# Performance work log

Measured on AMD Instinct MI355X. Metric: run time of the kernel, lower is better.

The kernel has to match this reference:

```python
import jax, jax.numpy as jnp
import numpy as np

B = 8192
D = 4096  # input_size == hidden_size (required by the module's forward)
H = 4096


def setup_inputs() -> dict:
    key = jax.random.key(0)
    ks = jax.random.split(key, 14)
    s = 0.02
    inp = {
        "input": jax.random.normal(ks[0], (B, D), dtype=jnp.float32),
        "hidden_state": jax.random.normal(ks[1], (B, H), dtype=jnp.float32),
        # torch nn.Linear weights: [out_features, in_features]
        "w_ir": jax.random.normal(ks[2], (H, D), dtype=jnp.float32) * s,
        "b_ir": jax.random.normal(ks[3], (H,), dtype=jnp.float32) * s,
        "w_iz": jax.random.normal(ks[4], (H, D), dtype=jnp.float32) * s,
        "b_iz": jax.random.normal(ks[5], (H,), dtype=jnp.float32) * s,
        "w_in": jax.random.normal(ks[6], (H, D), dtype=jnp.float32) * s,
        "b_in": jax.random.normal(ks[7], (H,), dtype=jnp.float32) * s,
        "w_hr": jax.random.normal(ks[8], (H, H), dtype=jnp.float32) * s,
        "b_hr": jax.random.normal(ks[9], (H,), dtype=jnp.float32) * s,
        "w_hz": jax.random.normal(ks[10], (H, H), dtype=jnp.float32) * s,
        "b_hz": jax.random.normal(ks[11], (H,), dtype=jnp.float32) * s,
        "w_hn": jax.random.normal(ks[12], (H, H), dtype=jnp.float32) * s,
        "b_hn": jax.random.normal(ks[13], (H,), dtype=jnp.float32) * s,
    }
    return inp


def reference(input, hidden_state, w_ir, b_ir, w_iz, b_iz, w_in, b_in,
              w_hr, b_hr, w_hz, b_hz, w_hn, b_hn):
    # NOTE: faithful to the source: ALL six gates are applied to `input`
    # (the hidden_* gates are also fed `input`, not hidden_state), and the
    # "new" gate uses sigmoid (not tanh).
    # Fuse the six small GEMMs into one batched GEMM: stack weights [6H, D].
    W = jnp.concatenate([w_ir, w_iz, w_in, w_hr, w_hz, w_hn], axis=0)  # [6H, D]
    bvec = jnp.concatenate([b_ir, b_iz, b_in, b_hr, b_hz, b_hn], axis=0)  # [6H]
    g = jnp.einsum('bd,od->bo', input, W) + bvec  # [B, 6H]
    ir, iz, inn, hr, hz, hn = jnp.split(g, 6, axis=-1)
    r = jax.nn.sigmoid(ir + hr)
    z = jax.nn.sigmoid(iz + hz)
    n = jax.nn.sigmoid(inn + r * hn)
    return (1.0 - z) * hidden_state + z * n
```

## Files before the change

### kernel.cpp

```cpp
#include <hip/hip_runtime.h>
#include <hip/hip_bf16.h>


#define THREADS 512
#define B_DIM 8192
#define D_DIM 4096
#define H_DIM 4096
#define BM 256
#define GBN 64
#define BK 32
#define NT (D_DIM / BK)
#define TBYTES 32768

#define WS_WR 0
#define WS_WZ 33554432
#define WS_WN 67108864
#define WS_WH 100663296
#define WS_A  134217728
#define WS_NEED 201326592ULL

typedef __attribute__((ext_vector_type(8))) short bf16x8;
typedef __attribute__((ext_vector_type(4))) float f32x4;
typedef __attribute__((ext_vector_type(4))) int i32x4;

__device__ __forceinline__ unsigned f2bf(float f) {
    union { float f; unsigned u; } v; v.f = f;
    return (v.u + 0x7FFFu + ((v.u >> 16) & 1u)) >> 16;
}
__device__ __forceinline__ unsigned pk(float a, float b) {
    return (f2bf(a) & 0xFFFFu) | (f2bf(b) << 16);
}
__device__ __forceinline__ i32x4 pack8(float4 x, float4 y) {
    i32x4 r;
    r[0] = (int)pk(x.x, x.y); r[1] = (int)pk(x.z, x.w);
    r[2] = (int)pk(y.x, y.y); r[3] = (int)pk(y.z, y.w);
    return r;
}
__device__ __forceinline__ float sigmoidf_(float x) {
    return 1.0f / (1.0f + __expf(-x));
}
__device__ __forceinline__ void gld16(const void* g, void* l) {
    __builtin_amdgcn_global_load_lds(
        (const __attribute__((address_space(1))) unsigned*)g,
        (__attribute__((address_space(3))) unsigned*)l, 16, 0, 0);
}

__global__ __launch_bounds__(256) void prep_w_t(
    const float* __restrict__ ir, const float* __restrict__ hr,
    const float* __restrict__ iz, const float* __restrict__ hz,
    const float* __restrict__ inw, const float* __restrict__ hn,
    char* __restrict__ wsbase)
{
    const int tx = threadIdx.x;
    const int R = tx & 15;
    const int c8loc = tx >> 4;
    const int bx = blockIdx.x;
    const int c8blk = bx & 31;
    const int hgrp = bx >> 5;
    const int gy = blockIdx.y;
    const int h  = hgrp * 16 + R;
    const int c8 = c8blk * 16 + c8loc;

    const float* s1 = (gy == 0) ? ir : (gy == 1) ? iz : (gy == 2) ? inw : hn;
    const size_t fi = ((size_t)h * 512 + c8) * 2;
    const float4* p1 = (const float4*)s1;
    float4 a0 = p1[fi], a1 = p1[fi + 1];
    if (gy < 2) {
        const float4* p2 = (const float4*)((gy == 0) ? hr : hz);
        a0 = a0 + p2[fi];
        a1 = a1 + p2[fi + 1];
    }
    const i32x4 v = pack8(a0, a1);
    const int hblk = h >> 6, nfr = (h >> 4) & 3;
    const int t = c8 >> 2, C = c8 & 3;
    const size_t addr = (size_t)gy * 33554432 + (size_t)hblk * 524288
                      + (size_t)t * 4096 + nfr * 1024 + C * 256 + R * 16;
    *(i32x4*)(wsbase + addr) = v;
}

__global__ __launch_bounds__(256) void prep_a_t(const float* __restrict__ in,
                                                char* __restrict__ abase)
{
    const int tx = threadIdx.x;
    const int R = tx & 15;
    const int c8loc = tx >> 4;
    const int bx = blockIdx.x;
    const int c8blk = bx & 31;
    const int bgrp = bx >> 5;
    const int b  = bgrp * 16 + R;
    const int c8 = c8blk * 16 + c8loc;

    const size_t fi = ((size_t)b * 512 + c8) * 2;
    const float4* p = (const float4*)in;
    const i32x4 v = pack8(p[fi], p[fi + 1]);
    const int bblk = b >> 8, mfr = (b >> 4) & 15;
    const int t = c8 >> 2, C = c8 & 3;
    const size_t addr = (size_t)bblk * 2097152 + (size_t)t * 16384
                      + mfr * 1024 + C * 256 + R * 16;
    *(i32x4*)(abase + addr) = v;
}

__global__ __launch_bounds__(THREADS, 2) void gru_bf16(
    const char* __restrict__ Abf, const char* __restrict__ Wr,
    const char* __restrict__ Wz, const char* __restrict__ Wn,
    const char* __restrict__ Wh,
    const float* __restrict__ hidden,
    const float* __restrict__ b_ir, const float* __restrict__ b_iz,
    const float* __restrict__ b_in, const float* __restrict__ b_hr,
    const float* __restrict__ b_hz, const float* __restrict__ b_hn,
    float* __restrict__ out)
{
    __shared__ __attribute__((aligned(128))) char smem[4 * TBYTES];

    const int tid  = threadIdx.x;
    const int lane = tid & 63;
    const int wid  = tid >> 6;
    const int wm   = wid >> 2;
    const int wn   = wid & 3;

    const int nb   = (int)blockIdx.x;
    const int bblk = nb & 31;
    const int hblk = nb >> 5;
    const int b0 = bblk * BM;
    const int h0 = hblk * GBN;

    const int gg = (wid >= 4) ? (wid - 4) : 0;
    const char* gW = (gg == 0) ? Wr : (gg == 1) ? Wz : (gg == 2) ? Wn : Wh;
    const char* psrc = (wid < 4)
        ? Abf + (size_t)bblk * 2097152 + (size_t)(4 * wid) * 1024 + (lane << 4)
        : gW + (size_t)hblk * 524288 + (lane << 4);
    const size_t pstep = (wid < 4) ? 16384 : 4096;
    const int dst = (wid < 4) ? (4 * wid) * 1024 : (16384 + gg * 4096);

    f32x4 acc[4][8];
#pragma unroll
    for (int g = 0; g < 4; ++g)
#pragma unroll
        for (int m = 0; m < 8; ++m) acc[g][m] = (f32x4)0.0f;

#define STAGE(x) do {                                                          \
        const char* s_ = psrc + (size_t)(x) * pstep;                           \
        char* l_ = smem + ((x) & 3) * TBYTES + dst;                            \
        gld16(s_, l_); gld16(s_ + 1024, l_ + 1024);                            \
        gld16(s_ + 2048, l_ + 2048); gld16(s_ + 3072, l_ + 3072);              \
    } while (0)

#define RD(dA_, dF_, x) do {                                                   \
        const char* cb_ = smem + ((x) & 3) * TBYTES;                           \
        _Pragma("unroll")                                                      \
        for (int mf = 0; mf < 8; ++mf)                                         \
            dA_[mf] = *(const bf16x8*)(cb_ + (wm * 8 + mf) * 1024 + (lane << 4)); \
        _Pragma("unroll")                                                      \
        for (int g = 0; g < 4; ++g)                                            \
            dF_[g] = *(const bf16x8*)(cb_ + 16384 + g * 4096 + wn * 1024 + (lane << 4)); \
    } while (0)

#define MM(acc_, a_, b_) acc_ = __builtin_amdgcn_mfma_f32_16x16x32_bf16(a_, b_, acc_, 0, 0, 0)

#define MFMA32(A_, F_) do {                                                    \
        __builtin_amdgcn_s_setprio(1);                                         \
        _Pragma("unroll")                                                      \
        for (int g = 0; g < 4; ++g)                                            \
            _Pragma("unroll")                                                  \
            for (int mf = 0; mf < 8; ++mf)                                     \
                MM(acc[g][mf], A_[mf], F_[g]);                                 \
        __builtin_amdgcn_s_setprio(0);                                         \
    } while (0)

#define SB0 __builtin_amdgcn_sched_barrier(0)

#define BODY(t, cA, cF, nA, nF) do {                                           \
        asm volatile("s_waitcnt lgkmcnt(0)" ::: "memory");                     \
        SB0;                                                                   \
        if ((t) + 3 < NT) STAGE((t) + 3);                                      \
        if ((t) + 1 < NT) RD(nA, nF, (t) + 1);                                 \
        MFMA32(cA, cF);                                                        \
        if ((t) <= NT - 4) { asm volatile("s_waitcnt vmcnt(4)" ::: "memory"); }\
        else               { asm volatile("s_waitcnt vmcnt(0)" ::: "memory"); }\
        SB0;                                                                   \
        __builtin_amdgcn_s_barrier();                                          \
    } while (0)

    bf16x8 a0[8], f0[4], a1[8], f1[4];

    STAGE(0); STAGE(1); STAGE(2);
    asm volatile("s_waitcnt vmcnt(4)" ::: "memory");
    SB0;
    __builtin_amdgcn_s_barrier();
    RD(a0, f0, 0);

#pragma unroll 1
    for (int t = 0; t < NT; t += 2) {
        BODY(t,     a0, f0, a1, f1);
        BODY(t + 1, a1, f1, a0, f0);
    }

    const int r4 = (lane >> 4) * 4;
    const int cn = lane & 15;
    {
        const int h = h0 + wn * 16 + cn;
        const float br = b_ir[h] + b_hr[h];
        const float bz = b_iz[h] + b_hz[h];
        const float bn = b_in[h];
        const float bh = b_hn[h];
#pragma unroll
        for (int m = 0; m < 8; ++m) {
            const int brow = b0 + wm * 128 + m * 16 + r4;
#pragma unroll
            for (int j = 0; j < 4; ++j) {
                const size_t idx = (size_t)(brow + j) * H_DIM + h;
                const float r = sigmoidf_(acc[0][m][j] + br);
                const float z = sigmoidf_(acc[1][m][j] + bz);
                const float n = sigmoidf_(acc[2][m][j] + bn + r * (acc[3][m][j] + bh));
                out[idx] = (1.0f - z) * hidden[idx] + z * n;
            }
        }
    }
#undef STAGE
#undef RD
#undef MM
#undef MFMA32
#undef SB0
#undef BODY
}

__global__ __launch_bounds__(THREADS, 2) void gru_fused_f32(
    const float* __restrict__ input, const float* __restrict__ hidden,
    const float* __restrict__ w_ir, const float* __restrict__ b_ir,
    const float* __restrict__ w_iz, const float* __restrict__ b_iz,
    const float* __restrict__ w_in, const float* __restrict__ b_in,
    const float* __restrict__ w_hr, const float* __restrict__ b_hr,
    const float* __restrict__ w_hz, const float* __restrict__ b_hz,
    const float* __restrict__ w_hn, const float* __restrict__ b_hn,
    float* __restrict__ out)
{
    __shared__ int smem[2 * 10240];
    const int tid  = threadIdx.x;
    const int lane = tid & 63;
    const int wid  = tid >> 6;
    const int wm   = wid >> 2;
    const int wn   = wid & 3;
    const int bblk = blockIdx.x & 63;
    const int hblk = blockIdx.x >> 6;
    const int b0 = bblk * 128;
    const int h0 = hblk * 128;
    const int srow = tid >> 2;
    const int sc   = tid & 3;
    const float4* gA  = (const float4*)(input + (size_t)(b0 + srow) * D_DIM + sc * 8);
    const size_t woff = (size_t)(h0 + srow) * D_DIM + sc * 8;
    const float4* gIr = (const float4*)(w_ir + woff);
    const float4* gHr = (const float4*)(w_hr + woff);
    const float4* gIz = (const float4*)(w_iz + woff);
    const float4* gHz = (const float4*)(w_hz + woff);
    const float4* gIn = (const float4*)(w_in + woff);
    const float4* gHn = (const float4*)(w_hn + woff);
    const int wr_ints = (srow >> 4) * 256 + ((sc * 16 + (srow & 15)) * 4);

    f32x4 accR[4][2], accZ[4][2], accN[4][2], accH[4][2];
#pragma unroll
    for (int mf = 0; mf < 4; ++mf)
#pragma unroll
        for (int nf = 0; nf < 2; ++nf) {
            accR[mf][nf] = (f32x4)0.0f; accZ[mf][nf] = (f32x4)0.0f;
            accN[mf][nf] = (f32x4)0.0f; accH[mf][nf] = (f32x4)0.0f;
        }
    float4 La0, La1, Lr0, Lr1, Lr2, Lr3, Lz0, Lz1, Lz2, Lz3, Ln0, Ln1, Lh0, Lh1;
#define LOADREGS(s) do { const int o = (s) * 8;                          \
        La0 = gA[o];  La1 = gA[o + 1];                                   \
        Lr0 = gIr[o]; Lr1 = gIr[o + 1]; Lr2 = gHr[o]; Lr3 = gHr[o + 1];  \
        Lz0 = gIz[o]; Lz1 = gIz[o + 1]; Lz2 = gHz[o]; Lz3 = gHz[o + 1];  \
        Ln0 = gIn[o]; Ln1 = gIn[o + 1];                                  \
        Lh0 = gHn[o]; Lh1 = gHn[o + 1]; } while (0)
#define WRITELDS(pp) do { const int wb = (pp) * 10240 + wr_ints;          \
        *(i32x4*)&smem[wb]        = pack8(La0, La1);                      \
        *(i32x4*)&smem[wb + 2048] = pack8(Lr0 + Lr2, Lr1 + Lr3);          \
        *(i32x4*)&smem[wb + 4096] = pack8(Lz0 + Lz2, Lz1 + Lz3);          \
        *(i32x4*)&smem[wb + 6144] = pack8(Ln0, Ln1);                      \
        *(i32x4*)&smem[wb + 8192] = pack8(Lh0, Lh1); } while (0)
#define COMPUTE(pp) do {                                                  \
        const int cb = (pp) * 10240;                                      \
        const bf16x8* Af = (const bf16x8*)&smem[cb];                      \
        const bf16x8* Br = (const bf16x8*)&smem[cb + 2048];               \
        const bf16x8* Bz = (const bf16x8*)&smem[cb + 4096];               \
        const bf16x8* Bn = (const bf16x8*)&smem[cb + 6144];               \
        const bf16x8* Bh = (const bf16x8*)&smem[cb + 8192];               \
        bf16x8 afr[4];                                                    \
        _Pragma("unroll")                                                 \
        for (int mf = 0; mf < 4; ++mf)                                    \
            afr[mf] = Af[(wm * 4 + mf) * 64 + lane];                      \
        _Pragma("unroll")                                                 \
        for (int nf = 0; nf < 2; ++nf) {                                  \
            const int bi = (wn * 2 + nf) * 64 + lane;                     \
            bf16x8 fr = Br[bi], fz = Bz[bi], fn = Bn[bi], fh = Bh[bi];    \
            _Pragma("unroll")                                             \
            for (int mf = 0; mf < 4; ++mf) {                              \
                accR[mf][nf] = __builtin_amdgcn_mfma_f32_16x16x32_bf16(afr[mf], fr, accR[mf][nf], 0, 0, 0); \
                accZ[mf][nf] = __builtin_amdgcn_mfma_f32_16x16x32_bf16(afr[mf], fz, accZ[mf][nf], 0, 0, 0); \
                accN[mf][nf] = __builtin_amdgcn_mfma_f32_16x16x32_bf16(afr[mf], fn, accN[mf][nf], 0, 0, 0); \
                accH[mf][nf] = __builtin_amdgcn_mfma_f32_16x16x32_bf16(afr[mf], fh, accH[mf][nf], 0, 0, 0); \
            }                                                             \
        } } while (0)
    LOADREGS(0);
    WRITELDS(0);
    __syncthreads();
#pragma unroll 1
    for (int s = 0; s < 128; ++s) {
        if (s + 1 < 128) LOADREGS(s + 1);
        COMPUTE(s & 1);
        if (s + 1 < 128) { WRITELDS((s + 1) & 1); __syncthreads(); }
    }
    const int r4 = (lane >> 4) * 4;
    const int cn = lane & 15;
#pragma unroll
    for (int nf = 0; nf < 2; ++nf) {
        const int h = h0 + wn * 32 + nf * 16 + cn;
        const float br = b_ir[h] + b_hr[h];
        const float bz = b_iz[h] + b_hz[h];
        const float bn = b_in[h];
        const float bh = b_hn[h];
#pragma unroll
        for (int mf = 0; mf < 4; ++mf) {
            const int brow = b0 + wm * 64 + mf * 16 + r4;
#pragma unroll
            for (int j = 0; j < 4; ++j) {
                const size_t idx = (size_t)(brow + j) * H_DIM + h;
                const float r = sigmoidf_(accR[mf][nf][j] + br);
                const float z = sigmoidf_(accZ[mf][nf][j] + bz);
                const float n = sigmoidf_(accN[mf][nf][j] + bn + r * (accH[mf][nf][j] + bh));
                out[idx] = (1.0f - z) * hidden[idx] + z * n;
            }
        }
    }
#undef LOADREGS
#undef WRITELDS
#undef COMPUTE
}

extern "C" void kernel_launch(void* const* d_in, const int* in_sizes, int n_in,
                              void* d_out, int out_size, void* d_ws, size_t ws_size,
                              hipStream_t stream) {
    const float* input  = (const float*)d_in[0];
    const float* hidden = (const float*)d_in[1];
    const float* w_ir = (const float*)d_in[2];  const float* b_ir = (const float*)d_in[3];
    const float* w_iz = (const float*)d_in[4];  const float* b_iz = (const float*)d_in[5];
    const float* w_in = (const float*)d_in[6];  const float* b_in = (const float*)d_in[7];
    const float* w_hr = (const float*)d_in[8];  const float* b_hr = (const float*)d_in[9];
    const float* w_hz = (const float*)d_in[10]; const float* b_hz = (const float*)d_in[11];
    const float* w_hn = (const float*)d_in[12]; const float* b_hn = (const float*)d_in[13];
    float* out = (float*)d_out;

    if (ws_size >= WS_NEED) {
        char* ws = (char*)d_ws;
        prep_w_t<<<dim3(8192, 4), dim3(256), 0, stream>>>(
            w_ir, w_hr, w_iz, w_hz, w_in, w_hn, ws);
        prep_a_t<<<dim3(16384), dim3(256), 0, stream>>>(input, ws + WS_A);
        gru_bf16<<<dim3((B_DIM / BM) * (H_DIM / GBN)), dim3(THREADS), 0, stream>>>(
            ws + WS_A, ws + WS_WR, ws + WS_WZ, ws + WS_WN, ws + WS_WH,
            hidden, b_ir, b_iz, b_in, b_hr, b_hz, b_hn, out);
    } else {
        gru_fused_f32<<<dim3(2048), dim3(THREADS), 0, stream>>>(
            input, hidden, w_ir, b_ir, w_iz, b_iz, w_in, b_in,
            w_hr, b_hr, w_hz, b_hz, w_hn, b_hn, out);
    }
}
```

Before: 1.023 ms.

## Shrink GEMM tile to 128 rows with 256-thread blocks and double-buffered LDS

Halves the batch tile per block and the thread count, with each wave now computing all 128 rows for its own column slice across the four gate groups. The deep four-stage LDS prefetch ring with register double-buffering is replaced by a two-stage buffer that waits for all global loads every K step. The A-operand prep kernel layout is adjusted to the new tile shape. This reduces LDS use and doubles the block count, at the cost of lower data reuse per block and less latency hiding.

```diff
diff --git a/kernel.cpp b/kernel.cpp
--- a/kernel.cpp
+++ b/kernel.cpp
@@ -2,15 +2,14 @@
 #include <hip/hip_bf16.h>
 
 
-#define THREADS 512
 #define B_DIM 8192
 #define D_DIM 4096
 #define H_DIM 4096
-#define BM 256
+#define BM 128
 #define GBN 64
 #define BK 32
 #define NT (D_DIM / BK)
-#define TBYTES 32768
+#define TBYTES 24576
 
 #define WS_WR 0
 #define WS_WZ 33554432
@@ -93,14 +92,14 @@
     const size_t fi = ((size_t)b * 512 + c8) * 2;
     const float4* p = (const float4*)in;
     const i32x4 v = pack8(p[fi], p[fi + 1]);
-    const int bblk = b >> 8, mfr = (b >> 4) & 15;
+    const int bblk = b >> 7, mfr = (b >> 4) & 7;
     const int t = c8 >> 2, C = c8 & 3;
-    const size_t addr = (size_t)bblk * 2097152 + (size_t)t * 16384
+    const size_t addr = (size_t)bblk * 1048576 + (size_t)t * 8192
                       + mfr * 1024 + C * 256 + R * 16;
     *(i32x4*)(abase + addr) = v;
 }
 
-__global__ __launch_bounds__(THREADS, 2) void gru_bf16(
+__global__ __launch_bounds__(256, 2) void gru_bf16(
     const char* __restrict__ Abf, const char* __restrict__ Wr,
     const char* __restrict__ Wz, const char* __restrict__ Wn,
     const char* __restrict__ Wh,
@@ -110,27 +109,39 @@
     const float* __restrict__ b_hz, const float* __restrict__ b_hn,
     float* __restrict__ out)
 {
-    __shared__ __attribute__((aligned(128))) char smem[4 * TBYTES];
+    __shared__ __attribute__((aligned(128))) char smem[2 * TBYTES];
 
     const int tid  = threadIdx.x;
     const int lane = tid & 63;
     const int wid  = tid >> 6;
-    const int wm   = wid >> 2;
-    const int wn   = wid & 3;
+    const int wn   = wid;
 
     const int nb   = (int)blockIdx.x;
-    const int bblk = nb & 31;
-    const int hblk = nb >> 5;
+    const int bblk = nb & 63;
+    const int hblk = nb >> 6;
     const int b0 = bblk * BM;
     const int h0 = hblk * GBN;
 
-    const int gg = (wid >= 4) ? (wid - 4) : 0;
-    const char* gW = (gg == 0) ? Wr : (gg == 1) ? Wz : (gg == 2) ? Wn : Wh;
-    const char* psrc = (wid < 4)
-        ? Abf + (size_t)bblk * 2097152 + (size_t)(4 * wid) * 1024 + (lane << 4)
-        : gW + (size_t)hblk * 524288 + (lane << 4);
-    const size_t pstep = (wid < 4) ? 16384 : 4096;
-    const int dst = (wid < 4) ? (4 * wid) * 1024 : (16384 + gg * 4096);
+    const char* sp[6];  int lo[6];  int kst[6];
+#pragma unroll
+    for (int i = 0; i < 6; ++i) {
+        const int f = wid * 6 + i;
+        if (f < 8) {
+            sp[i]  = Abf + (size_t)bblk * 1048576 + f * 1024;
+            lo[i]  = f * 1024;
+            kst[i] = 8192;
+        } else {
+            const int bf = f - 8, g = bf >> 2, nf = bf & 3;
+            const char* W = (g == 0) ? Wr : (g == 1) ? Wz : (g == 2) ? Wn : Wh;
+            sp[i]  = W + (size_t)hblk * 524288 + nf * 1024;
+            lo[i]  = 8192 + g * 4096 + nf * 1024;
+            kst[i] = 4096;
+        }
+        sp[i] += (size_t)lane * 16;
+    }
+    const char* rp[6];
+#pragma unroll
+    for (int i = 0; i < 6; ++i) rp[i] = sp[i] + kst[i];
 
     f32x4 acc[4][8];
 #pragma unroll
@@ -138,61 +149,46 @@
 #pragma unroll
         for (int m = 0; m < 8; ++m) acc[g][m] = (f32x4)0.0f;
 
-#define STAGE(x) do {                                                          \
-        const char* s_ = psrc + (size_t)(x) * pstep;                           \
-        char* l_ = smem + ((x) & 3) * TBYTES + dst;                            \
-        gld16(s_, l_); gld16(s_ + 1024, l_ + 1024);                            \
-        gld16(s_ + 2048, l_ + 2048); gld16(s_ + 3072, l_ + 3072);              \
-    } while (0)
-
-#define RD(dA_, dF_, x) do {                                                   \
-        const char* cb_ = smem + ((x) & 3) * TBYTES;                           \
-        _Pragma("unroll")                                                      \
-        for (int mf = 0; mf < 8; ++mf)                                         \
-            dA_[mf] = *(const bf16x8*)(cb_ + (wm * 8 + mf) * 1024 + (lane << 4)); \
-        _Pragma("unroll")                                                      \
-        for (int g = 0; g < 4; ++g)                                            \
-            dF_[g] = *(const bf16x8*)(cb_ + 16384 + g * 4096 + wn * 1024 + (lane << 4)); \
-    } while (0)
-
 #define MM(acc_, a_, b_) acc_ = __builtin_amdgcn_mfma_f32_16x16x32_bf16(a_, b_, acc_, 0, 0, 0)
 
-#define MFMA32(A_, F_) do {                                                    \
-        __builtin_amdgcn_s_setprio(1);                                         \
-        _Pragma("unroll")                                                      \
-        for (int g = 0; g < 4; ++g)                                            \
-            _Pragma("unroll")                                                  \
-            for (int mf = 0; mf < 8; ++mf)                                     \
-                MM(acc[g][mf], A_[mf], F_[g]);                                 \
-        __builtin_amdgcn_s_setprio(0);                                         \
-    } while (0)
-
-#define SB0 __builtin_amdgcn_sched_barrier(0)
-
-#define BODY(t, cA, cF, nA, nF) do {                                           \
-        asm volatile("s_waitcnt lgkmcnt(0)" ::: "memory");                     \
-        SB0;                                                                   \
-        if ((t) + 3 < NT) STAGE((t) + 3);                                      \
-        if ((t) + 1 < NT) RD(nA, nF, (t) + 1);                                 \
-        MFMA32(cA, cF);                                                        \
-        if ((t) <= NT - 4) { asm volatile("s_waitcnt vmcnt(4)" ::: "memory"); }\
-        else               { asm volatile("s_waitcnt vmcnt(0)" ::: "memory"); }\
-        SB0;                                                                   \
-        __builtin_amdgcn_s_barrier();                                          \
-    } while (0)
-
-    bf16x8 a0[8], f0[4], a1[8], f1[4];
-
-    STAGE(0); STAGE(1); STAGE(2);
-    asm volatile("s_waitcnt vmcnt(4)" ::: "memory");
-    SB0;
+#pragma unroll
+    for (int i = 0; i < 6; ++i) gld16(sp[i], smem + lo[i]);
+    asm volatile("s_waitcnt vmcnt(0)" ::: "memory");
+    __builtin_amdgcn_sched_barrier(0);
     __builtin_amdgcn_s_barrier();
-    RD(a0, f0, 0);
 
 #pragma unroll 1
-    for (int t = 0; t < NT; t += 2) {
-        BODY(t,     a0, f0, a1, f1);
-        BODY(t + 1, a1, f1, a0, f0);
+    for (int t = 0; t < NT; ++t) {
+        const char* cb = smem + (t & 1) * TBYTES;
+        char* d = smem + ((t + 1) & 1) * TBYTES;
+        const bool stg = (t + 1 < NT);
+
+        if (stg) {
+#pragma unroll
+            for (int i = 0; i < 6; ++i) {
+                gld16(rp[i], d + lo[i]);
+                rp[i] += kst[i];
+            }
+        }
+        bf16x8 af[8], fb[4];
+#pragma unroll
+        for (int mf = 0; mf < 8; ++mf)
+            af[mf] = *(const bf16x8*)(cb + mf * 1024 + (lane << 4));
+#pragma unroll
+        for (int g = 0; g < 4; ++g)
+            fb[g] = *(const bf16x8*)(cb + 8192 + g * 4096 + wn * 1024 + (lane << 4));
+
+        __builtin_amdgcn_s_setprio(1);
+#pragma unroll
+        for (int g = 0; g < 4; ++g)
+#pragma unroll
+            for (int mf = 0; mf < 8; ++mf)
+                MM(acc[g][mf], af[mf], fb[g]);
+        __builtin_amdgcn_s_setprio(0);
+
+        if (stg) { asm volatile("s_waitcnt vmcnt(0)" ::: "memory"); }
+        __builtin_amdgcn_sched_barrier(0);
+        __builtin_amdgcn_s_barrier();
     }
 
     const int r4 = (lane >> 4) * 4;
@@ -205,7 +201,7 @@
         const float bh = b_hn[h];
 #pragma unroll
         for (int m = 0; m < 8; ++m) {
-            const int brow = b0 + wm * 128 + m * 16 + r4;
+            const int brow = b0 + m * 16 + r4;
 #pragma unroll
             for (int j = 0; j < 4; ++j) {
                 const size_t idx = (size_t)(brow + j) * H_DIM + h;
@@ -216,15 +212,10 @@
             }
         }
     }
-#undef STAGE
-#undef RD
 #undef MM
-#undef MFMA32
-#undef SB0
-#undef BODY
-}
-
-__global__ __launch_bounds__(THREADS, 2) void gru_fused_f32(
+}
+
+__global__ __launch_bounds__(512, 2) void gru_fused_f32(
     const float* __restrict__ input, const float* __restrict__ hidden,
     const float* __restrict__ w_ir, const float* __restrict__ b_ir,
     const float* __restrict__ w_iz, const float* __restrict__ b_iz,
@@ -354,11 +345,11 @@
         prep_w_t<<<dim3(8192, 4), dim3(256), 0, stream>>>(
             w_ir, w_hr, w_iz, w_hz, w_in, w_hn, ws);
         prep_a_t<<<dim3(16384), dim3(256), 0, stream>>>(input, ws + WS_A);
-        gru_bf16<<<dim3((B_DIM / BM) * (H_DIM / GBN)), dim3(THREADS), 0, stream>>>(
+        gru_bf16<<<dim3((B_DIM / BM) * (H_DIM / GBN)), dim3(256), 0, stream>>>(
             ws + WS_A, ws + WS_WR, ws + WS_WZ, ws + WS_WN, ws + WS_WH,
             hidden, b_ir, b_iz, b_in, b_hr, b_hz, b_hn, out);
     } else {
-        gru_fused_f32<<<dim3(2048), dim3(THREADS), 0, stream>>>(
+        gru_fused_f32<<<dim3(2048), dim3(512), 0, stream>>>(
             input, hidden, w_ir, b_ir, w_iz, b_iz, w_in, b_in,
             w_hr, b_hr, w_hz, b_hz, w_hn, b_hn, out);
     }
```

Result: slower. 1.051 ms, median of 2 (+2.7%).
